# Performance work log

Hardware: AMD Instinct MI355X
Metric: run time of the kernel (lower is better)

## Reference

```python
import jax, jax.numpy as jnp
import numpy as np

B, DM, E, P, K = 8192, 512, 4, 1024, 2
F = DM * E  # fused_input_dim = 2048


def setup_inputs() -> dict:
    key = jax.random.key(0)
    ks = jax.random.split(key, 8)
    return {
        "x_mod0": jax.random.normal(ks[0], (B, DM), jnp.float32),
        "x_mod1": jax.random.normal(ks[1], (B, DM), jnp.float32),
        "x_mod2": jax.random.normal(ks[2], (B, DM), jnp.float32),
        "x_mod3": jax.random.normal(ks[3], (B, DM), jnp.float32),
        "label": jax.random.normal(ks[4], (B, P), jnp.float32),
        "Wg": jax.random.normal(ks[5], (E, F), jnp.float32) * (1.0 / np.sqrt(F)),
        "We": jax.random.normal(ks[6], (E, F, P), jnp.float32) * (1.0 / np.sqrt(F)),
        "be": jax.random.normal(ks[7], (E, P), jnp.float32) * 0.01,
        "topk": K,
    }


def reference(x_mod0, x_mod1, x_mod2, x_mod3, label, Wg, We, be, topk):
    # fused = cat(modalities, dim=1)  -> [B, F]
    fused = jnp.concatenate([x_mod0, x_mod1, x_mod2, x_mod3], axis=1)
    # gate_scores = softmax(Linear(fused))  (Linear weight is [out,in], no bias)
    gate_scores = jax.nn.softmax(fused @ Wg.T, axis=-1)  # [B, E]
    top_k_values, top_k_indices = jax.lax.top_k(gate_scores, topk)  # [B, K]
    # Dense equivalent of per-sample expert dispatch: run every expert,
    # then gather the top-k expert outputs per token and weighted-sum them.
    all_out = jnp.einsum("bf,efp->bep", fused, We) + be  # [B, E, P]
    gathered = jnp.take_along_axis(all_out, top_k_indices[:, :, None], axis=1)  # [B, K, P]
    preds = jnp.sum(gathered * top_k_values[:, :, None], axis=1)  # [B, P]
    # loss_fn = MSE against x['label']
    loss = jnp.mean((preds - label) ** 2)
    return (loss, preds)
```

## Files before the change

kernel.cpp:

```cpp
#include <hip/hip_runtime.h>
#include <stdint.h>

#define Bsz  8192
#define DMOD 512
#define NE   4
#define NP   1024
#define NF   2048
#define BM   160
#define MAXTILES 57

typedef float  f32x4  __attribute__((ext_vector_type(4)));
typedef __bf16 bf16x8 __attribute__((ext_vector_type(8)));
typedef unsigned short u16x8 __attribute__((ext_vector_type(8)));

typedef __attribute__((address_space(3))) void       lds_void;
typedef const __attribute__((address_space(1))) void glb_void;
#define GLOAD16(gp, lp) \
  __builtin_amdgcn_global_load_lds((glb_void*)(gp), (lds_void*)(lp), 16, 0, 0)

__device__ __forceinline__ unsigned short f32_bf16(float f) {
  unsigned int u = __float_as_uint(f);
  u += 0x7FFFu + ((u >> 16) & 1u);
  return (unsigned short)(u >> 16);
}

__global__ __launch_bounds__(256) void gate_kernel(
    const float* __restrict__ x0, const float* __restrict__ x1,
    const float* __restrict__ x2, const float* __restrict__ x3,
    const float* __restrict__ Wg,
    float* __restrict__ gw, int* __restrict__ pair)
{
  __shared__ float sred[4][4];
  const int b   = blockIdx.x;
  const int tid = threadIdx.x;
  const int f   = tid * 8;
  const float* xm  = (f < 1024) ? (f < 512 ? x0 : x1) : (f < 1536 ? x2 : x3);
  const float* src = xm + (size_t)b * DMOD + (f & 511);
  float4 v0 = *(const float4*)src;
  float4 v1 = *(const float4*)(src + 4);

  float d[4];
  #pragma unroll
  for (int e = 0; e < 4; ++e) {
    const float* w = Wg + e * NF + f;
    d[e] = v0.x * w[0] + v0.y * w[1] + v0.z * w[2] + v0.w * w[3]
         + v1.x * w[4] + v1.y * w[5] + v1.z * w[6] + v1.w * w[7];
  }
  #pragma unroll
  for (int off = 32; off; off >>= 1) {
    #pragma unroll
    for (int e = 0; e < 4; ++e) d[e] += __shfl_xor(d[e], off);
  }
  if ((tid & 63) == 0) {
    #pragma unroll
    for (int e = 0; e < 4; ++e) sred[tid >> 6][e] = d[e];
  }
  __syncthreads();
  if (tid == 0) {
    float a0 = sred[0][0] + sred[1][0] + sred[2][0] + sred[3][0];
    float a1 = sred[0][1] + sred[1][1] + sred[2][1] + sred[3][1];
    float a2 = sred[0][2] + sred[1][2] + sred[2][2] + sred[3][2];
    float a3 = sred[0][3] + sred[1][3] + sred[2][3] + sred[3][3];
    float m  = fmaxf(fmaxf(a0, a1), fmaxf(a2, a3));
    float e0 = expf(a0 - m), e1 = expf(a1 - m), e2 = expf(a2 - m), e3 = expf(a3 - m);
    float inv = 1.f / (e0 + e1 + e2 + e3);
    float p0 = e0 * inv, p1 = e1 * inv, p2 = e2 * inv, p3 = e3 * inv;
    int i1 = 0; float b1 = a0;
    if (a1 > b1) { b1 = a1; i1 = 1; }
    if (a2 > b1) { b1 = a2; i1 = 2; }
    if (a3 > b1) { b1 = a3; i1 = 3; }
    int i2 = -1; float b2 = -3.4e38f;
    if (i1 != 0 && a0 > b2) { b2 = a0; i2 = 0; }
    if (i1 != 1 && a1 > b2) { b2 = a1; i2 = 1; }
    if (i1 != 2 && a2 > b2) { b2 = a2; i2 = 2; }
    if (i1 != 3 && a3 > b2) { b2 = a3; i2 = 3; }
    gw[(size_t)b * 4 + 0] = (i1 == 0 || i2 == 0) ? p0 : 0.f;
    gw[(size_t)b * 4 + 1] = (i1 == 1 || i2 == 1) ? p1 : 0.f;
    gw[(size_t)b * 4 + 2] = (i1 == 2 || i2 == 2) ? p2 : 0.f;
    gw[(size_t)b * 4 + 3] = (i1 == 3 || i2 == 3) ? p3 : 0.f;
    int lo = min(i1, i2), hi = max(i1, i2);
    pair[b] = (lo == 0) ? (hi - 1) : (lo == 1) ? (hi + 1) : 5;
  }
}

__global__ __launch_bounds__(256) void we_transpose(
    const float* __restrict__ We, unsigned short* __restrict__ WeT)
{
  __shared__ float t[64][65];
  const int e  = blockIdx.z;
  const int tf = blockIdx.x * 64;
  const int tp = blockIdx.y * 64;
  const int t4 = threadIdx.x * 4;
  const float* src = We + ((size_t)e * NF + tf) * NP + tp;
  #pragma unroll
  for (int i = 0; i < 4; ++i) {
    int li = i * 1024 + t4;
    int r = li >> 6, c = li & 63;
    float4 v = *(const float4*)(src + (size_t)r * NP + c);
    t[c][r] = v.x; t[c+1][r] = v.y; t[c+2][r] = v.z; t[c+3][r] = v.w;
  }
  __syncthreads();
  unsigned short* dst = WeT + ((size_t)e * NP + tp) * NF + tf;
  #pragma unroll
  for (int i = 0; i < 4; ++i) {
    int li = i * 1024 + t4;
    int r = li >> 6, c = li & 63;
    ushort4 o;
    o.x = f32_bf16(t[r][c]);   o.y = f32_bf16(t[r][c+1]);
    o.z = f32_bf16(t[r][c+2]); o.w = f32_bf16(t[r][c+3]);
    *(ushort4*)(dst + (size_t)r * NF + c) = o;
  }
}

__global__ __launch_bounds__(256) void bucket_scan(
    const int* __restrict__ pair, int* __restrict__ ridx,
    int4* __restrict__ tiletab, int* __restrict__ ntiles,
    double* __restrict__ lossAcc)
{
  __shared__ int cntS[256][6];
  __shared__ int baseS[6];
  const int tid = threadIdx.x;
  int c[6] = {0, 0, 0, 0, 0, 0};
  for (int i = 0; i < 32; ++i) {
    const int code = pair[tid * 32 + i];
    #pragma unroll
    for (int b = 0; b < 6; ++b) c[b] += (code == b) ? 1 : 0;
  }
  #pragma unroll
  for (int b = 0; b < 6; ++b) cntS[tid][b] = c[b];
  __syncthreads();
  if (tid < 6) {
    int run = 0;
    for (int i = 0; i < 256; ++i) { const int v = cntS[i][tid]; cntS[i][tid] = run; run += v; }
    baseS[tid] = run;
  }
  __syncthreads();
  if (tid == 0) {
    const int e1t[6] = {0, 0, 0, 1, 1, 2};
    const int e2t[6] = {1, 2, 3, 2, 3, 3};
    int base[6];
    int off = 0, nt = 0;
    for (int b = 0; b < 6; ++b) {
      base[b] = off;
      const int cb = baseS[b];
      for (int i = 0; i < cb; i += BM)
        tiletab[nt++] = make_int4(off + i, min(BM, cb - i), e1t[b], e2t[b]);
      off += cb;
    }
    *ntiles = nt;
    *lossAcc = 0.0;
    #pragma unroll
    for (int b = 0; b < 6; ++b) baseS[b] = base[b];
  }
  __syncthreads();
  int pos[6];
  #pragma unroll
  for (int b = 0; b < 6; ++b) pos[b] = baseS[b] + cntS[tid][b];
  for (int i = 0; i < 32; ++i) {
    const int r = tid * 32 + i;
    const int code = pair[r];
    #pragma unroll
    for (int b = 0; b < 6; ++b)
      if (code == b) { ridx[pos[b]] = r; ++pos[b]; }
  }
}

__global__ __launch_bounds__(256) void permute_cvt(
    const float* __restrict__ x0, const float* __restrict__ x1,
    const float* __restrict__ x2, const float* __restrict__ x3,
    const int* __restrict__ ridx, unsigned short* __restrict__ fusedP)
{
  const int pos = blockIdx.x;
  const int r   = ridx[pos];
  const int tid = threadIdx.x;
  const int f   = tid * 8;
  const float* xm  = (f < 1024) ? (f < 512 ? x0 : x1) : (f < 1536 ? x2 : x3);
  const float* src = xm + (size_t)r * DMOD + (f & 511);
  float4 v0 = *(const float4*)src;
  float4 v1 = *(const float4*)(src + 4);
  u16x8 o;
  o[0] = f32_bf16(v0.x); o[1] = f32_bf16(v0.y); o[2] = f32_bf16(v0.z); o[3] = f32_bf16(v0.w);
  o[4] = f32_bf16(v1.x); o[5] = f32_bf16(v1.y); o[6] = f32_bf16(v1.z); o[7] = f32_bf16(v1.w);
  *(u16x8*)(fusedP + (size_t)pos * NF + f) = o;
}

__global__ __launch_bounds__(256, 2) void moe_gemm(
    const unsigned short* __restrict__ fusedP,
    const unsigned short* __restrict__ WeT,
    const float* __restrict__ gw,
    const float* __restrict__ be,
    const float* __restrict__ label,
    const int* __restrict__ ntilesP,
    const int4* __restrict__ tiletab,
    const int* __restrict__ ridx,
    float* __restrict__ out,
    double* __restrict__ lossAcc)
{
  const int bid  = (int)blockIdx.x;
  const int swz  = (bid & 7) * 57 + (bid >> 3);
  const int tile = swz >> 3;
  if (tile >= *ntilesP) return;
  const int pcol = (swz & 7) * 128;

  __shared__ __align__(16) unsigned short As[2][BM * 64];
  __shared__ __align__(16) unsigned short Bs[2][128 * 64];
  __shared__ int   ridxS[BM];
  __shared__ float gwS[BM][2];
  __shared__ float red[4];

  const int4 te     = tiletab[tile];
  const int rowbase = te.x;
  const int vcount  = te.y;
  const int e1      = te.z;
  const int e2      = te.w;

  const int tid  = threadIdx.x;
  const int l    = tid & 63;
  const int wave = tid >> 6;
  const int wr   = wave >> 1;
  const int wc   = wave & 1;
  const int lrow = l & 15;
  const int g4   = l >> 4;
  const int lr8  = l >> 3;
  const int lc8  = l & 7;
  const int schA = lc8 ^ lr8;

  if (tid < BM) {
    const int ri = ridx[rowbase + min(tid, vcount - 1)];
    ridxS[tid]  = ri;
    gwS[tid][0] = gw[(size_t)ri * 4 + e1];
    gwS[tid][1] = gw[(size_t)ri * 4 + e2];
  }
  __syncthreads();

  int rowA[5];
  #pragma unroll
  for (int i = 0; i < 5; ++i)
    rowA[i] = rowbase + min(wave * 40 + i * 8 + lr8, vcount - 1);

  f32x4 accT[5][4], accE[5][4];
  #pragma unroll
  for (int m = 0; m < 5; ++m)
    #pragma unroll
    for (int n = 0; n < 4; ++n) {
      accT[m][n] = f32x4{0.f, 0.f, 0.f, 0.f};
      accE[m][n] = f32x4{0.f, 0.f, 0.f, 0.f};
    }

  auto STAGE = [&](int t, int buf) {
    const int e  = (t >> 5) ? e2 : e1;
    const int k0 = (t & 31) << 6;
    const unsigned short* Bg = WeT + ((size_t)e * NP + pcol) * NF + k0;
    #pragma unroll
    for (int i = 0; i < 5; ++i) {
      const int r0 = wave * 40 + i * 8;
      GLOAD16(fusedP + (size_t)rowA[i] * NF + k0 + schA * 8, (char*)(&As[buf][r0 * 64]));
    }
    #pragma unroll
    for (int i = 0; i < 4; ++i) {
      const int r0 = wave * 32 + i * 8;
      GLOAD16(Bg + (size_t)(r0 + lr8) * NF + schA * 8, (char*)(&Bs[buf][r0 * 64]));
    }
  };

  auto COMPUTE = [&](int buf) {
    #pragma unroll
    for (int ks = 0; ks < 2; ++ks) {
      bf16x8 af[5], bfr[4];
      #pragma unroll
      for (int m = 0; m < 5; ++m) {
        const int fr = wr * 80 + m * 16 + lrow;
        const int ch = ((g4 + ks * 4) ^ (fr & 7)) * 8;
        af[m] = __builtin_bit_cast(bf16x8, *(const u16x8*)(&As[buf][fr * 64 + ch]));
      }
      #pragma unroll
      for (int n = 0; n < 4; ++n) {
        const int fr = wc * 64 + n * 16 + lrow;
        const int ch = ((g4 + ks * 4) ^ (fr & 7)) * 8;
        bfr[n] = __builtin_bit_cast(bf16x8, *(const u16x8*)(&Bs[buf][fr * 64 + ch]));
      }
      #pragma unroll
      for (int m = 0; m < 5; ++m)
        #pragma unroll
        for (int n = 0; n < 4; ++n)
          accE[m][n] = __builtin_amdgcn_mfma_f32_16x16x32_bf16(af[m], bfr[n], accE[m][n], 0, 0, 0);
    }
  };

  auto FOLD = [&](int ei) {
    #pragma unroll
    for (int m = 0; m < 5; ++m)
      #pragma unroll
      for (int r = 0; r < 4; ++r) {
        const float wv = gwS[wr * 80 + m * 16 + g4 * 4 + r][ei];
        #pragma unroll
        for (int n = 0; n < 4; ++n) {
          accT[m][n][r] += wv * accE[m][n][r];
          accE[m][n][r] = 0.f;
        }
      }
  };

  STAGE(0, 0);
  STAGE(1, 1);

  #pragma unroll 1
  for (int t = 0; t < 64; ++t) {
    const int buf = t & 1;
    if (t == 63) asm volatile("s_waitcnt vmcnt(0)" ::: "memory");
    else         asm volatile("s_waitcnt vmcnt(9)" ::: "memory");
    __builtin_amdgcn_s_barrier();
    COMPUTE(buf);
    if ((t & 31) == 31) FOLD(t >> 5);
    __builtin_amdgcn_sched_barrier(0);
    __builtin_amdgcn_s_barrier();
    if (t < 62) STAGE(t + 2, buf);
  }

  float lsum = 0.f;
  #pragma unroll
  for (int m = 0; m < 5; ++m) {
    #pragma unroll
    for (int r = 0; r < 4; ++r) {
      const int lrowi = wr * 80 + m * 16 + g4 * 4 + r;
      const bool valid = lrowi < vcount;
      const int grow = ridxS[lrowi];
      const float w1 = gwS[lrowi][0];
      const float w2 = gwS[lrowi][1];
      #pragma unroll
      for (int n = 0; n < 4; ++n) {
        const int gcol = pcol + wc * 64 + n * 16 + lrow;
        float bias = w1 * be[e1 * NP + gcol] + w2 * be[e2 * NP + gcol];
        float pred = accT[m][n][r] + bias;
        if (valid) {
          out[1 + (size_t)grow * NP + gcol] = pred;
          float d = pred - label[(size_t)grow * NP + gcol];
          lsum += d * d;
        }
      }
    }
  }
  #pragma unroll
  for (int off = 32; off; off >>= 1) lsum += __shfl_xor(lsum, off);
  if (l == 0) red[wave] = lsum;
  __syncthreads();
  if (tid == 0) {
    double s = (double)red[0] + (double)red[1] + (double)red[2] + (double)red[3];
    atomicAdd(lossAcc, s);
  }
}

__global__ void finalize_kernel(const double* __restrict__ lossAcc, float* __restrict__ out) {
  out[0] = (float)(*lossAcc * (1.0 / ((double)Bsz * (double)NP)));
}

extern "C" void kernel_launch(void* const* d_in, const int* in_sizes, int n_in,
                              void* d_out, int out_size, void* d_ws, size_t ws_size,
                              hipStream_t stream) {
  const float* x0    = (const float*)d_in[0];
  const float* x1    = (const float*)d_in[1];
  const float* x2    = (const float*)d_in[2];
  const float* x3    = (const float*)d_in[3];
  const float* label = (const float*)d_in[4];
  const float* Wg    = (const float*)d_in[5];
  const float* We    = (const float*)d_in[6];
  const float* be    = (const float*)d_in[7];
  float* out = (float*)d_out;

  char* ws = (char*)d_ws;
  unsigned short* WeT    = (unsigned short*)ws;
  unsigned short* fusedP = (unsigned short*)(ws + ((size_t)16 << 20));
  float*  gw      = (float*)(ws + ((size_t)48 << 20));
  char*   misc    = ws + ((size_t)49 << 20);
  double* lossAcc = (double*)(misc + 0);
  int*    ntiles  = (int*)(misc + 64);
  int4*   tiletab = (int4*)(misc + 256);
  int*    pair    = (int*)(misc + 4096);
  int*    ridx    = (int*)(misc + 4096 + 32768);

  gate_kernel<<<dim3(Bsz), 256, 0, stream>>>(x0, x1, x2, x3, Wg, gw, pair);
  bucket_scan<<<dim3(1), 256, 0, stream>>>(pair, ridx, tiletab, ntiles, lossAcc);
  permute_cvt<<<dim3(Bsz), 256, 0, stream>>>(x0, x1, x2, x3, ridx, fusedP);
  we_transpose<<<dim3(NF / 64, NP / 64, NE), 256, 0, stream>>>(We, WeT);
  moe_gemm<<<dim3(MAXTILES * 8), 256, 0, stream>>>(
      fusedP, WeT, gw, be, label, ntiles, tiletab, ridx, out, lossAcc);
  finalize_kernel<<<1, 1, 0, stream>>>(lossAcc, out);
}
```

Before: 171.0 us.

## Pre-scale tokens by gate weights and run single K=4096 GEMM per tile

Merges the We transpose into the gate kernel launch so both run in one grid. A new permute kernel writes two bf16 copies of each token, each pre-multiplied by one of its two gate weights. This lets the new 512-thread GEMM use one accumulator over a concatenated K of 4096 (two experts) instead of separate per-expert accumulators followed by a weighted combine. The cost is twice the permuted-activation bytes written and read, plus rounding of the scaled activations to bf16. The new path runs only when the workspace is large enough; otherwise the old pipeline is kept.

```diff
diff --git a/kernel.cpp b/kernel.cpp
--- a/kernel.cpp
+++ b/kernel.cpp
@@ -24,98 +24,99 @@
   return (unsigned short)(u >> 16);
 }
 
-__global__ __launch_bounds__(256) void gate_kernel(
+__global__ __launch_bounds__(256) void gate_tr(
     const float* __restrict__ x0, const float* __restrict__ x1,
     const float* __restrict__ x2, const float* __restrict__ x3,
-    const float* __restrict__ Wg,
-    float* __restrict__ gw, int* __restrict__ pair)
+    const float* __restrict__ Wg, const float* __restrict__ We,
+    float* __restrict__ gw, int* __restrict__ pair,
+    unsigned short* __restrict__ WeT)
 {
   __shared__ float sred[4][4];
-  const int b   = blockIdx.x;
+  __shared__ float tsh[64][65];
   const int tid = threadIdx.x;
-  const int f   = tid * 8;
-  const float* xm  = (f < 1024) ? (f < 512 ? x0 : x1) : (f < 1536 ? x2 : x3);
-  const float* src = xm + (size_t)b * DMOD + (f & 511);
-  float4 v0 = *(const float4*)src;
-  float4 v1 = *(const float4*)(src + 4);
-
-  float d[4];
-  #pragma unroll
-  for (int e = 0; e < 4; ++e) {
-    const float* w = Wg + e * NF + f;
-    d[e] = v0.x * w[0] + v0.y * w[1] + v0.z * w[2] + v0.w * w[3]
-         + v1.x * w[4] + v1.y * w[5] + v1.z * w[6] + v1.w * w[7];
-  }
-  #pragma unroll
-  for (int off = 32; off; off >>= 1) {
-    #pragma unroll
-    for (int e = 0; e < 4; ++e) d[e] += __shfl_xor(d[e], off);
-  }
-  if ((tid & 63) == 0) {
-    #pragma unroll
-    for (int e = 0; e < 4; ++e) sred[tid >> 6][e] = d[e];
-  }
-  __syncthreads();
-  if (tid == 0) {
-    float a0 = sred[0][0] + sred[1][0] + sred[2][0] + sred[3][0];
-    float a1 = sred[0][1] + sred[1][1] + sred[2][1] + sred[3][1];
-    float a2 = sred[0][2] + sred[1][2] + sred[2][2] + sred[3][2];
-    float a3 = sred[0][3] + sred[1][3] + sred[2][3] + sred[3][3];
-    float m  = fmaxf(fmaxf(a0, a1), fmaxf(a2, a3));
-    float e0 = expf(a0 - m), e1 = expf(a1 - m), e2 = expf(a2 - m), e3 = expf(a3 - m);
-    float inv = 1.f / (e0 + e1 + e2 + e3);
-    float p0 = e0 * inv, p1 = e1 * inv, p2 = e2 * inv, p3 = e3 * inv;
-    int i1 = 0; float b1 = a0;
-    if (a1 > b1) { b1 = a1; i1 = 1; }
-    if (a2 > b1) { b1 = a2; i1 = 2; }
-    if (a3 > b1) { b1 = a3; i1 = 3; }
-    int i2 = -1; float b2 = -3.4e38f;
-    if (i1 != 0 && a0 > b2) { b2 = a0; i2 = 0; }
-    if (i1 != 1 && a1 > b2) { b2 = a1; i2 = 1; }
-    if (i1 != 2 && a2 > b2) { b2 = a2; i2 = 2; }
-    if (i1 != 3 && a3 > b2) { b2 = a3; i2 = 3; }
-    gw[(size_t)b * 4 + 0] = (i1 == 0 || i2 == 0) ? p0 : 0.f;
-    gw[(size_t)b * 4 + 1] = (i1 == 1 || i2 == 1) ? p1 : 0.f;
-    gw[(size_t)b * 4 + 2] = (i1 == 2 || i2 == 2) ? p2 : 0.f;
-    gw[(size_t)b * 4 + 3] = (i1 == 3 || i2 == 3) ? p3 : 0.f;
-    int lo = min(i1, i2), hi = max(i1, i2);
-    pair[b] = (lo == 0) ? (hi - 1) : (lo == 1) ? (hi + 1) : 5;
-  }
-}
-
-__global__ __launch_bounds__(256) void we_transpose(
-    const float* __restrict__ We, unsigned short* __restrict__ WeT)
-{
-  __shared__ float t[64][65];
-  const int e  = blockIdx.z;
-  const int tf = blockIdx.x * 64;
-  const int tp = blockIdx.y * 64;
-  const int t4 = threadIdx.x * 4;
-  const float* src = We + ((size_t)e * NF + tf) * NP + tp;
-  #pragma unroll
-  for (int i = 0; i < 4; ++i) {
-    int li = i * 1024 + t4;
-    int r = li >> 6, c = li & 63;
-    float4 v = *(const float4*)(src + (size_t)r * NP + c);
-    t[c][r] = v.x; t[c+1][r] = v.y; t[c+2][r] = v.z; t[c+3][r] = v.w;
-  }
-  __syncthreads();
-  unsigned short* dst = WeT + ((size_t)e * NP + tp) * NF + tf;
-  #pragma unroll
-  for (int i = 0; i < 4; ++i) {
-    int li = i * 1024 + t4;
-    int r = li >> 6, c = li & 63;
-    ushort4 o;
-    o.x = f32_bf16(t[r][c]);   o.y = f32_bf16(t[r][c+1]);
-    o.z = f32_bf16(t[r][c+2]); o.w = f32_bf16(t[r][c+3]);
-    *(ushort4*)(dst + (size_t)r * NF + c) = o;
+
+  if ((int)blockIdx.x < Bsz) {
+    const int b = blockIdx.x;
+    const int f = tid * 8;
+    const float* xm  = (f < 1024) ? (f < 512 ? x0 : x1) : (f < 1536 ? x2 : x3);
+    const float* src = xm + (size_t)b * DMOD + (f & 511);
+    float4 v0 = *(const float4*)src;
+    float4 v1 = *(const float4*)(src + 4);
+    float d[4];
+    #pragma unroll
+    for (int e = 0; e < 4; ++e) {
+      const float* w = Wg + e * NF + f;
+      d[e] = v0.x * w[0] + v0.y * w[1] + v0.z * w[2] + v0.w * w[3]
+           + v1.x * w[4] + v1.y * w[5] + v1.z * w[6] + v1.w * w[7];
+    }
+    #pragma unroll
+    for (int off = 32; off; off >>= 1) {
+      #pragma unroll
+      for (int e = 0; e < 4; ++e) d[e] += __shfl_xor(d[e], off);
+    }
+    if ((tid & 63) == 0) {
+      #pragma unroll
+      for (int e = 0; e < 4; ++e) sred[tid >> 6][e] = d[e];
+    }
+    __syncthreads();
+    if (tid == 0) {
+      float a0 = sred[0][0] + sred[1][0] + sred[2][0] + sred[3][0];
+      float a1 = sred[0][1] + sred[1][1] + sred[2][1] + sred[3][1];
+      float a2 = sred[0][2] + sred[1][2] + sred[2][2] + sred[3][2];
+      float a3 = sred[0][3] + sred[1][3] + sred[2][3] + sred[3][3];
+      float m  = fmaxf(fmaxf(a0, a1), fmaxf(a2, a3));
+      float e0 = expf(a0 - m), e1 = expf(a1 - m), e2 = expf(a2 - m), e3 = expf(a3 - m);
+      float inv = 1.f / (e0 + e1 + e2 + e3);
+      float p0 = e0 * inv, p1 = e1 * inv, p2 = e2 * inv, p3 = e3 * inv;
+      int i1 = 0; float b1 = a0;
+      if (a1 > b1) { b1 = a1; i1 = 1; }
+      if (a2 > b1) { b1 = a2; i1 = 2; }
+      if (a3 > b1) { b1 = a3; i1 = 3; }
+      int i2 = -1; float b2 = -3.4e38f;
+      if (i1 != 0 && a0 > b2) { b2 = a0; i2 = 0; }
+      if (i1 != 1 && a1 > b2) { b2 = a1; i2 = 1; }
+      if (i1 != 2 && a2 > b2) { b2 = a2; i2 = 2; }
+      if (i1 != 3 && a3 > b2) { b2 = a3; i2 = 3; }
+      gw[(size_t)b * 4 + 0] = (i1 == 0 || i2 == 0) ? p0 : 0.f;
+      gw[(size_t)b * 4 + 1] = (i1 == 1 || i2 == 1) ? p1 : 0.f;
+      gw[(size_t)b * 4 + 2] = (i1 == 2 || i2 == 2) ? p2 : 0.f;
+      gw[(size_t)b * 4 + 3] = (i1 == 3 || i2 == 3) ? p3 : 0.f;
+      int lo = min(i1, i2), hi = max(i1, i2);
+      pair[b] = (lo == 0) ? (hi - 1) : (lo == 1) ? (hi + 1) : 5;
+    }
+  } else {
+    const int tb = (int)blockIdx.x - Bsz;
+    const int e  = tb >> 9;
+    const int rem = tb & 511;
+    const int tf = (rem & 31) * 64;
+    const int tp = (rem >> 5) * 64;
+    const int t4 = tid * 4;
+    const float* src = We + ((size_t)e * NF + tf) * NP + tp;
+    #pragma unroll
+    for (int i = 0; i < 4; ++i) {
+      int li = i * 1024 + t4;
+      int r = li >> 6, c = li & 63;
+      float4 v = *(const float4*)(src + (size_t)r * NP + c);
+      tsh[c][r] = v.x; tsh[c+1][r] = v.y; tsh[c+2][r] = v.z; tsh[c+3][r] = v.w;
+    }
+    __syncthreads();
+    unsigned short* dst = WeT + ((size_t)e * NP + tp) * NF + tf;
+    #pragma unroll
+    for (int i = 0; i < 4; ++i) {
+      int li = i * 1024 + t4;
+      int r = li >> 6, c = li & 63;
+      ushort4 o;
+      o.x = f32_bf16(tsh[r][c]);   o.y = f32_bf16(tsh[r][c+1]);
+      o.z = f32_bf16(tsh[r][c+2]); o.w = f32_bf16(tsh[r][c+3]);
+      *(ushort4*)(dst + (size_t)r * NF + c) = o;
+    }
   }
 }
 
 __global__ __launch_bounds__(256) void bucket_scan(
     const int* __restrict__ pair, int* __restrict__ ridx,
-    int4* __restrict__ tiletab, int* __restrict__ ntiles,
-    double* __restrict__ lossAcc)
+    int4* __restrict__ tiletab, int4* __restrict__ bucketTab,
+    int* __restrict__ ntiles, double* __restrict__ lossAcc)
 {
   __shared__ int cntS[256][6];
   __shared__ int baseS[6];
@@ -143,6 +144,7 @@
     for (int b = 0; b < 6; ++b) {
       base[b] = off;
       const int cb = baseS[b];
+      bucketTab[b] = make_int4(off, cb, e1t[b], e2t[b]);
       for (int i = 0; i < cb; i += BM)
         tiletab[nt++] = make_int4(off + i, min(BM, cb - i), e1t[b], e2t[b]);
       off += cb;
@@ -163,6 +165,39 @@
     for (int b = 0; b < 6; ++b)
       if (code == b) { ridx[pos[b]] = r; ++pos[b]; }
   }
+}
+
+__global__ __launch_bounds__(256) void permute_scale(
+    const float* __restrict__ x0, const float* __restrict__ x1,
+    const float* __restrict__ x2, const float* __restrict__ x3,
+    const int* __restrict__ ridx, const float* __restrict__ gw,
+    const int4* __restrict__ bucketTab, unsigned short* __restrict__ fusedP)
+{
+  const int pos = blockIdx.x;
+  int e1 = 0, e2 = 1;
+  #pragma unroll
+  for (int b = 0; b < 6; ++b) {
+    const int4 bt = bucketTab[b];
+    if (pos >= bt.x && pos < bt.x + bt.y) { e1 = bt.z; e2 = bt.w; }
+  }
+  const int ri = ridx[pos];
+  const float w1 = gw[(size_t)ri * 4 + e1];
+  const float w2 = gw[(size_t)ri * 4 + e2];
+  const int tid = threadIdx.x;
+  const int f   = tid * 8;
+  const float* xm  = (f < 1024) ? (f < 512 ? x0 : x1) : (f < 1536 ? x2 : x3);
+  const float* src = xm + (size_t)ri * DMOD + (f & 511);
+  float4 v0 = *(const float4*)src;
+  float4 v1 = *(const float4*)(src + 4);
+  float v[8] = {v0.x, v0.y, v0.z, v0.w, v1.x, v1.y, v1.z, v1.w};
+  u16x8 o1, o2;
+  #pragma unroll
+  for (int j = 0; j < 8; ++j) {
+    o1[j] = f32_bf16(v[j] * w1);
+    o2[j] = f32_bf16(v[j] * w2);
+  }
+  *(u16x8*)(fusedP + (size_t)pos * NF + f) = o1;
+  *(u16x8*)(fusedP + ((size_t)Bsz + pos) * NF + f) = o2;
 }
 
 __global__ __launch_bounds__(256) void permute_cvt(
@@ -184,7 +219,7 @@
   *(u16x8*)(fusedP + (size_t)pos * NF + f) = o;
 }
 
-__global__ __launch_bounds__(256, 2) void moe_gemm(
+__global__ __launch_bounds__(512, 4) void moe_gemm_v8(
     const unsigned short* __restrict__ fusedP,
     const unsigned short* __restrict__ WeT,
     const float* __restrict__ gw,
@@ -206,6 +241,156 @@
   __shared__ __align__(16) unsigned short Bs[2][128 * 64];
   __shared__ int   ridxS[BM];
   __shared__ float gwS[BM][2];
+  __shared__ float red[8];
+
+  const int4 te     = tiletab[tile];
+  const int rowbase = te.x;
+  const int vcount  = te.y;
+  const int e1      = te.z;
+  const int e2      = te.w;
+
+  const int tid  = threadIdx.x;
+  const int l    = tid & 63;
+  const int wave = tid >> 6;
+  const int wr   = wave >> 2;
+  const int wc   = wave & 3;
+  const int lrow = l & 15;
+  const int g4   = l >> 4;
+  const int lr8  = l >> 3;
+  const int lc8  = l & 7;
+  const int schA = lc8 ^ lr8;
+
+  if (tid < BM) {
+    const int ri = ridx[rowbase + min(tid, vcount - 1)];
+    ridxS[tid]  = ri;
+    gwS[tid][0] = gw[(size_t)ri * 4 + e1];
+    gwS[tid][1] = gw[(size_t)ri * 4 + e2];
+  }
+  __syncthreads();
+
+  f32x4 accT[5][2];
+  #pragma unroll
+  for (int m = 0; m < 5; ++m)
+    #pragma unroll
+    for (int n = 0; n < 2; ++n) accT[m][n] = f32x4{0.f, 0.f, 0.f, 0.f};
+
+  auto STAGE = [&](int t, int buf) {
+    const int h  = t >> 5;
+    const int k0 = (t & 31) << 6;
+    const unsigned short* Ag = fusedP + (size_t)h * ((size_t)Bsz * NF) + k0;
+    const unsigned short* Bg = WeT + ((size_t)(h ? e2 : e1) * NP + pcol) * NF + k0;
+    #pragma unroll
+    for (int s = 0; s < 5; ++s) {
+      if (s == 4 && wave >= 4) continue;
+      const int idx = wave + s * 8;
+      if (idx < 20) {
+        const int r0  = idx * 8;
+        const int row = rowbase + min(r0 + lr8, vcount - 1);
+        GLOAD16(Ag + (size_t)row * NF + schA * 8, (char*)(&As[buf][r0 * 64]));
+      } else {
+        const int r0 = (idx - 20) * 8;
+        GLOAD16(Bg + (size_t)(r0 + lr8) * NF + schA * 8, (char*)(&Bs[buf][r0 * 64]));
+      }
+    }
+  };
+
+  auto COMPUTE = [&](int buf) {
+    #pragma unroll
+    for (int ks = 0; ks < 2; ++ks) {
+      bf16x8 af[5], bfr[2];
+      #pragma unroll
+      for (int m = 0; m < 5; ++m) {
+        const int fr = wr * 80 + m * 16 + lrow;
+        const int ch = ((g4 + ks * 4) ^ (fr & 7)) * 8;
+        af[m] = __builtin_bit_cast(bf16x8, *(const u16x8*)(&As[buf][fr * 64 + ch]));
+      }
+      #pragma unroll
+      for (int n = 0; n < 2; ++n) {
+        const int fr = wc * 32 + n * 16 + lrow;
+        const int ch = ((g4 + ks * 4) ^ (fr & 7)) * 8;
+        bfr[n] = __builtin_bit_cast(bf16x8, *(const u16x8*)(&Bs[buf][fr * 64 + ch]));
+      }
+      #pragma unroll
+      for (int m = 0; m < 5; ++m)
+        #pragma unroll
+        for (int n = 0; n < 2; ++n)
+          accT[m][n] = __builtin_amdgcn_mfma_f32_16x16x32_bf16(af[m], bfr[n], accT[m][n], 0, 0, 0);
+    }
+  };
+
+  STAGE(0, 0);
+  STAGE(1, 1);
+
+  #pragma unroll 1
+  for (int t = 0; t < 64; ++t) {
+    const int buf = t & 1;
+    if (t == 63)          { asm volatile("s_waitcnt vmcnt(0)" ::: "memory"); }
+    else if (wave < 4)    { asm volatile("s_waitcnt vmcnt(5)" ::: "memory"); }
+    else                  { asm volatile("s_waitcnt vmcnt(4)" ::: "memory"); }
+    __builtin_amdgcn_s_barrier();
+    COMPUTE(buf);
+    __builtin_amdgcn_sched_barrier(0);
+    __builtin_amdgcn_s_barrier();
+    if (t < 62) STAGE(t + 2, buf);
+  }
+
+  float lsum = 0.f;
+  #pragma unroll
+  for (int m = 0; m < 5; ++m) {
+    #pragma unroll
+    for (int r = 0; r < 4; ++r) {
+      const int lrowi = wr * 80 + m * 16 + g4 * 4 + r;
+      const bool valid = lrowi < vcount;
+      const int grow = ridxS[lrowi];
+      const float w1 = gwS[lrowi][0];
+      const float w2 = gwS[lrowi][1];
+      #pragma unroll
+      for (int n = 0; n < 2; ++n) {
+        const int gcol = pcol + wc * 32 + n * 16 + lrow;
+        float bias = w1 * be[e1 * NP + gcol] + w2 * be[e2 * NP + gcol];
+        float pred = accT[m][n][r] + bias;
+        if (valid) {
+          out[1 + (size_t)grow * NP + gcol] = pred;
+          float d = pred - label[(size_t)grow * NP + gcol];
+          lsum += d * d;
+        }
+      }
+    }
+  }
+  #pragma unroll
+  for (int off = 32; off; off >>= 1) lsum += __shfl_xor(lsum, off);
+  if (l == 0) red[wave] = lsum;
+  __syncthreads();
+  if (tid == 0) {
+    double s = 0.0;
+    #pragma unroll
+    for (int w = 0; w < 8; ++w) s += (double)red[w];
+    atomicAdd(lossAcc, s);
+  }
+}
+
+__global__ __launch_bounds__(256, 2) void moe_gemm_r7(
+    const unsigned short* __restrict__ fusedP,
+    const unsigned short* __restrict__ WeT,
+    const float* __restrict__ gw,
+    const float* __restrict__ be,
+    const float* __restrict__ label,
+    const int* __restrict__ ntilesP,
+    const int4* __restrict__ tiletab,
+    const int* __restrict__ ridx,
+    float* __restrict__ out,
+    double* __restrict__ lossAcc)
+{
+  const int bid  = (int)blockIdx.x;
+  const int swz  = (bid & 7) * 57 + (bid >> 3);
+  const int tile = swz >> 3;
+  if (tile >= *ntilesP) return;
+  const int pcol = (swz & 7) * 128;
+
+  __shared__ __align__(16) unsigned short As[2][BM * 64];
+  __shared__ __align__(16) unsigned short Bs[2][128 * 64];
+  __shared__ int   ridxS[BM];
+  __shared__ float gwS[BM][2];
   __shared__ float red[4];
 
   const int4 te     = tiletab[tile];
@@ -366,23 +551,45 @@
   const float* We    = (const float*)d_in[6];
   const float* be    = (const float*)d_in[7];
   float* out = (float*)d_out;
-
   char* ws = (char*)d_ws;
-  unsigned short* WeT    = (unsigned short*)ws;
-  unsigned short* fusedP = (unsigned short*)(ws + ((size_t)16 << 20));
-  float*  gw      = (float*)(ws + ((size_t)48 << 20));
-  char*   misc    = ws + ((size_t)49 << 20);
-  double* lossAcc = (double*)(misc + 0);
-  int*    ntiles  = (int*)(misc + 64);
-  int4*   tiletab = (int4*)(misc + 256);
-  int*    pair    = (int*)(misc + 4096);
-  int*    ridx    = (int*)(misc + 4096 + 32768);
-
-  gate_kernel<<<dim3(Bsz), 256, 0, stream>>>(x0, x1, x2, x3, Wg, gw, pair);
-  bucket_scan<<<dim3(1), 256, 0, stream>>>(pair, ridx, tiletab, ntiles, lossAcc);
-  permute_cvt<<<dim3(Bsz), 256, 0, stream>>>(x0, x1, x2, x3, ridx, fusedP);
-  we_transpose<<<dim3(NF / 64, NP / 64, NE), 256, 0, stream>>>(We, WeT);
-  moe_gemm<<<dim3(MAXTILES * 8), 256, 0, stream>>>(
-      fusedP, WeT, gw, be, label, ntiles, tiletab, ridx, out, lossAcc);
-  finalize_kernel<<<1, 1, 0, stream>>>(lossAcc, out);
-}
+
+  const bool bigWs = ws_size >= ((size_t)82 << 20);
+
+  if (bigWs) {
+    unsigned short* WeT    = (unsigned short*)ws;
+    unsigned short* fusedP = (unsigned short*)(ws + ((size_t)16 << 20));
+    char*   misc    = ws + ((size_t)80 << 20);
+    double* lossAcc = (double*)(misc + 0);
+    int*    ntiles  = (int*)(misc + 64);
+    int4*   tiletab = (int4*)(misc + 256);
+    int4*   bucketTab = (int4*)(misc + 2048);
+    int*    pair    = (int*)(misc + 4096);
+    int*    ridx    = (int*)(misc + 4096 + 32768);
+    float*  gw      = (float*)(misc + 4096 + 65536);
+
+    gate_tr<<<dim3(Bsz + 2048), 256, 0, stream>>>(x0, x1, x2, x3, Wg, We, gw, pair, WeT);
+    bucket_scan<<<dim3(1), 256, 0, stream>>>(pair, ridx, tiletab, bucketTab, ntiles, lossAcc);
+    permute_scale<<<dim3(Bsz), 256, 0, stream>>>(x0, x1, x2, x3, ridx, gw, bucketTab, fusedP);
+    moe_gemm_v8<<<dim3(MAXTILES * 8), 512, 0, stream>>>(
+        fusedP, WeT, gw, be, label, ntiles, tiletab, ridx, out, lossAcc);
+    finalize_kernel<<<1, 1, 0, stream>>>(lossAcc, out);
+  } else {
+    unsigned short* WeT    = (unsigned short*)ws;
+    unsigned short* fusedP = (unsigned short*)(ws + ((size_t)16 << 20));
+    float*  gw      = (float*)(ws + ((size_t)48 << 20));
+    char*   misc    = ws + ((size_t)49 << 20);
+    double* lossAcc = (double*)(misc + 0);
+    int*    ntiles  = (int*)(misc + 64);
+    int4*   tiletab = (int4*)(misc + 256);
+    int4*   bucketTab = (int4*)(misc + 2048);
+    int*    pair    = (int*)(misc + 4096);
+    int*    ridx    = (int*)(misc + 4096 + 32768);
+
+    gate_tr<<<dim3(Bsz + 2048), 256, 0, stream>>>(x0, x1, x2, x3, Wg, We, gw, pair, WeT);
+    bucket_scan<<<dim3(1), 256, 0, stream>>>(pair, ridx, tiletab, bucketTab, ntiles, lossAcc);
+    permute_cvt<<<dim3(Bsz), 256, 0, stream>>>(x0, x1, x2, x3, ridx, fusedP);
+    moe_gemm_r7<<<dim3(MAXTILES * 8), 256, 0, stream>>>(
+        fusedP, WeT, gw, be, label, ntiles, tiletab, ridx, out, lossAcc);
+    finalize_kernel<<<1, 1, 0, stream>>>(lossAcc, out);
+  }
+}
```

Result: faster. 161.2 us (-5.7%).

## Fuse gate, bf16 conversion and We transpose; compute both experts concurrently in GEMM

Applied to the files above, without the earlier changes.

The gate kernel, the activation bf16 conversion and the We transpose now run as one launch, and the separate permute kernel is removed. The GEMM now gathers rows through ridx directly from the unpermuted bf16 activations. The GEMM moves to 512 threads with K-step 32 and keeps two accumulator sets, one per expert, each multiplied against the same A fragment. This replaces the sequential two-expert K loop and its fold step. The aim is to cut launches and a full activation copy and to reuse A loads across both experts, at the cost of doubled B traffic per step, scattered row reads and a different pipeline depth.

```diff
diff --git a/kernel.cpp b/kernel.cpp
--- a/kernel.cpp
+++ b/kernel.cpp
@@ -24,91 +24,97 @@
   return (unsigned short)(u >> 16);
 }
 
-__global__ __launch_bounds__(256) void gate_kernel(
+__global__ __launch_bounds__(256) void gate_fuse(
     const float* __restrict__ x0, const float* __restrict__ x1,
     const float* __restrict__ x2, const float* __restrict__ x3,
-    const float* __restrict__ Wg,
-    float* __restrict__ gw, int* __restrict__ pair)
+    const float* __restrict__ Wg, const float* __restrict__ We,
+    float* __restrict__ gw, int* __restrict__ pair,
+    unsigned short* __restrict__ fusedB, unsigned short* __restrict__ WeT)
 {
   __shared__ float sred[4][4];
-  const int b   = blockIdx.x;
+  __shared__ float tsh[64][65];
   const int tid = threadIdx.x;
-  const int f   = tid * 8;
-  const float* xm  = (f < 1024) ? (f < 512 ? x0 : x1) : (f < 1536 ? x2 : x3);
-  const float* src = xm + (size_t)b * DMOD + (f & 511);
-  float4 v0 = *(const float4*)src;
-  float4 v1 = *(const float4*)(src + 4);
-
-  float d[4];
-  #pragma unroll
-  for (int e = 0; e < 4; ++e) {
-    const float* w = Wg + e * NF + f;
-    d[e] = v0.x * w[0] + v0.y * w[1] + v0.z * w[2] + v0.w * w[3]
-         + v1.x * w[4] + v1.y * w[5] + v1.z * w[6] + v1.w * w[7];
-  }
-  #pragma unroll
-  for (int off = 32; off; off >>= 1) {
-    #pragma unroll
-    for (int e = 0; e < 4; ++e) d[e] += __shfl_xor(d[e], off);
-  }
-  if ((tid & 63) == 0) {
-    #pragma unroll
-    for (int e = 0; e < 4; ++e) sred[tid >> 6][e] = d[e];
-  }
-  __syncthreads();
-  if (tid == 0) {
-    float a0 = sred[0][0] + sred[1][0] + sred[2][0] + sred[3][0];
-    float a1 = sred[0][1] + sred[1][1] + sred[2][1] + sred[3][1];
-    float a2 = sred[0][2] + sred[1][2] + sred[2][2] + sred[3][2];
-    float a3 = sred[0][3] + sred[1][3] + sred[2][3] + sred[3][3];
-    float m  = fmaxf(fmaxf(a0, a1), fmaxf(a2, a3));
-    float e0 = expf(a0 - m), e1 = expf(a1 - m), e2 = expf(a2 - m), e3 = expf(a3 - m);
-    float inv = 1.f / (e0 + e1 + e2 + e3);
-    float p0 = e0 * inv, p1 = e1 * inv, p2 = e2 * inv, p3 = e3 * inv;
-    int i1 = 0; float b1 = a0;
-    if (a1 > b1) { b1 = a1; i1 = 1; }
-    if (a2 > b1) { b1 = a2; i1 = 2; }
-    if (a3 > b1) { b1 = a3; i1 = 3; }
-    int i2 = -1; float b2 = -3.4e38f;
-    if (i1 != 0 && a0 > b2) { b2 = a0; i2 = 0; }
-    if (i1 != 1 && a1 > b2) { b2 = a1; i2 = 1; }
-    if (i1 != 2 && a2 > b2) { b2 = a2; i2 = 2; }
-    if (i1 != 3 && a3 > b2) { b2 = a3; i2 = 3; }
-    gw[(size_t)b * 4 + 0] = (i1 == 0 || i2 == 0) ? p0 : 0.f;
-    gw[(size_t)b * 4 + 1] = (i1 == 1 || i2 == 1) ? p1 : 0.f;
-    gw[(size_t)b * 4 + 2] = (i1 == 2 || i2 == 2) ? p2 : 0.f;
-    gw[(size_t)b * 4 + 3] = (i1 == 3 || i2 == 3) ? p3 : 0.f;
-    int lo = min(i1, i2), hi = max(i1, i2);
-    pair[b] = (lo == 0) ? (hi - 1) : (lo == 1) ? (hi + 1) : 5;
-  }
-}
-
-__global__ __launch_bounds__(256) void we_transpose(
-    const float* __restrict__ We, unsigned short* __restrict__ WeT)
-{
-  __shared__ float t[64][65];
-  const int e  = blockIdx.z;
-  const int tf = blockIdx.x * 64;
-  const int tp = blockIdx.y * 64;
-  const int t4 = threadIdx.x * 4;
-  const float* src = We + ((size_t)e * NF + tf) * NP + tp;
-  #pragma unroll
-  for (int i = 0; i < 4; ++i) {
-    int li = i * 1024 + t4;
-    int r = li >> 6, c = li & 63;
-    float4 v = *(const float4*)(src + (size_t)r * NP + c);
-    t[c][r] = v.x; t[c+1][r] = v.y; t[c+2][r] = v.z; t[c+3][r] = v.w;
-  }
-  __syncthreads();
-  unsigned short* dst = WeT + ((size_t)e * NP + tp) * NF + tf;
-  #pragma unroll
-  for (int i = 0; i < 4; ++i) {
-    int li = i * 1024 + t4;
-    int r = li >> 6, c = li & 63;
-    ushort4 o;
-    o.x = f32_bf16(t[r][c]);   o.y = f32_bf16(t[r][c+1]);
-    o.z = f32_bf16(t[r][c+2]); o.w = f32_bf16(t[r][c+3]);
-    *(ushort4*)(dst + (size_t)r * NF + c) = o;
+
+  if ((int)blockIdx.x < Bsz) {
+    const int b = blockIdx.x;
+    const int f = tid * 8;
+    const float* xm  = (f < 1024) ? (f < 512 ? x0 : x1) : (f < 1536 ? x2 : x3);
+    const float* src = xm + (size_t)b * DMOD + (f & 511);
+    float4 v0 = *(const float4*)src;
+    float4 v1 = *(const float4*)(src + 4);
+    u16x8 o;
+    o[0] = f32_bf16(v0.x); o[1] = f32_bf16(v0.y); o[2] = f32_bf16(v0.z); o[3] = f32_bf16(v0.w);
+    o[4] = f32_bf16(v1.x); o[5] = f32_bf16(v1.y); o[6] = f32_bf16(v1.z); o[7] = f32_bf16(v1.w);
+    *(u16x8*)(fusedB + (size_t)b * NF + f) = o;
+
+    float d[4];
+    #pragma unroll
+    for (int e = 0; e < 4; ++e) {
+      const float* w = Wg + e * NF + f;
+      d[e] = v0.x * w[0] + v0.y * w[1] + v0.z * w[2] + v0.w * w[3]
+           + v1.x * w[4] + v1.y * w[5] + v1.z * w[6] + v1.w * w[7];
+    }
+    #pragma unroll
+    for (int off = 32; off; off >>= 1) {
+      #pragma unroll
+      for (int e = 0; e < 4; ++e) d[e] += __shfl_xor(d[e], off);
+    }
+    if ((tid & 63) == 0) {
+      #pragma unroll
+      for (int e = 0; e < 4; ++e) sred[tid >> 6][e] = d[e];
+    }
+    __syncthreads();
+    if (tid == 0) {
+      float a0 = sred[0][0] + sred[1][0] + sred[2][0] + sred[3][0];
+      float a1 = sred[0][1] + sred[1][1] + sred[2][1] + sred[3][1];
+      float a2 = sred[0][2] + sred[1][2] + sred[2][2] + sred[3][2];
+      float a3 = sred[0][3] + sred[1][3] + sred[2][3] + sred[3][3];
+      float m  = fmaxf(fmaxf(a0, a1), fmaxf(a2, a3));
+      float e0 = expf(a0 - m), e1 = expf(a1 - m), e2 = expf(a2 - m), e3 = expf(a3 - m);
+      float inv = 1.f / (e0 + e1 + e2 + e3);
+      float p0 = e0 * inv, p1 = e1 * inv, p2 = e2 * inv, p3 = e3 * inv;
+      int i1 = 0; float b1 = a0;
+      if (a1 > b1) { b1 = a1; i1 = 1; }
+      if (a2 > b1) { b1 = a2; i1 = 2; }
+      if (a3 > b1) { b1 = a3; i1 = 3; }
+      int i2 = -1; float b2 = -3.4e38f;
+      if (i1 != 0 && a0 > b2) { b2 = a0; i2 = 0; }
+      if (i1 != 1 && a1 > b2) { b2 = a1; i2 = 1; }
+      if (i1 != 2 && a2 > b2) { b2 = a2; i2 = 2; }
+      if (i1 != 3 && a3 > b2) { b2 = a3; i2 = 3; }
+      gw[(size_t)b * 4 + 0] = (i1 == 0 || i2 == 0) ? p0 : 0.f;
+      gw[(size_t)b * 4 + 1] = (i1 == 1 || i2 == 1) ? p1 : 0.f;
+      gw[(size_t)b * 4 + 2] = (i1 == 2 || i2 == 2) ? p2 : 0.f;
+      gw[(size_t)b * 4 + 3] = (i1 == 3 || i2 == 3) ? p3 : 0.f;
+      int lo = min(i1, i2), hi = max(i1, i2);
+      pair[b] = (lo == 0) ? (hi - 1) : (lo == 1) ? (hi + 1) : 5;
+    }
+  } else {
+    const int tb = (int)blockIdx.x - Bsz;
+    const int e  = tb >> 9;
+    const int rem = tb & 511;
+    const int tf = (rem & 31) * 64;
+    const int tp = (rem >> 5) * 64;
+    const int t4 = tid * 4;
+    const float* src = We + ((size_t)e * NF + tf) * NP + tp;
+    #pragma unroll
+    for (int i = 0; i < 4; ++i) {
+      int li = i * 1024 + t4;
+      int r = li >> 6, c = li & 63;
+      float4 v = *(const float4*)(src + (size_t)r * NP + c);
+      tsh[c][r] = v.x; tsh[c+1][r] = v.y; tsh[c+2][r] = v.z; tsh[c+3][r] = v.w;
+    }
+    __syncthreads();
+    unsigned short* dst = WeT + ((size_t)e * NP + tp) * NF + tf;
+    #pragma unroll
+    for (int i = 0; i < 4; ++i) {
+      int li = i * 1024 + t4;
+      int r = li >> 6, c = li & 63;
+      ushort4 o;
+      o.x = f32_bf16(tsh[r][c]);   o.y = f32_bf16(tsh[r][c+1]);
+      o.z = f32_bf16(tsh[r][c+2]); o.w = f32_bf16(tsh[r][c+3]);
+      *(ushort4*)(dst + (size_t)r * NF + c) = o;
+    }
   }
 }
 
@@ -165,27 +171,8 @@
   }
 }
 
-__global__ __launch_bounds__(256) void permute_cvt(
-    const float* __restrict__ x0, const float* __restrict__ x1,
-    const float* __restrict__ x2, const float* __restrict__ x3,
-    const int* __restrict__ ridx, unsigned short* __restrict__ fusedP)
-{
-  const int pos = blockIdx.x;
-  const int r   = ridx[pos];
-  const int tid = threadIdx.x;
-  const int f   = tid * 8;
-  const float* xm  = (f < 1024) ? (f < 512 ? x0 : x1) : (f < 1536 ? x2 : x3);
-  const float* src = xm + (size_t)r * DMOD + (f & 511);
-  float4 v0 = *(const float4*)src;
-  float4 v1 = *(const float4*)(src + 4);
-  u16x8 o;
-  o[0] = f32_bf16(v0.x); o[1] = f32_bf16(v0.y); o[2] = f32_bf16(v0.z); o[3] = f32_bf16(v0.w);
-  o[4] = f32_bf16(v1.x); o[5] = f32_bf16(v1.y); o[6] = f32_bf16(v1.z); o[7] = f32_bf16(v1.w);
-  *(u16x8*)(fusedP + (size_t)pos * NF + f) = o;
-}
-
-__global__ __launch_bounds__(256, 2) void moe_gemm(
-    const unsigned short* __restrict__ fusedP,
+__global__ __launch_bounds__(512, 4) void moe_gemm_db(
+    const unsigned short* __restrict__ fusedB,
     const unsigned short* __restrict__ WeT,
     const float* __restrict__ gw,
     const float* __restrict__ be,
@@ -202,11 +189,12 @@
   if (tile >= *ntilesP) return;
   const int pcol = (swz & 7) * 128;
 
-  __shared__ __align__(16) unsigned short As[2][BM * 64];
-  __shared__ __align__(16) unsigned short Bs[2][128 * 64];
+  __shared__ __align__(16) unsigned short As[2][BM * 32];
+  __shared__ __align__(16) unsigned short B1s[2][128 * 32];
+  __shared__ __align__(16) unsigned short B2s[2][128 * 32];
   __shared__ int   ridxS[BM];
   __shared__ float gwS[BM][2];
-  __shared__ float red[4];
+  __shared__ float red[8];
 
   const int4 te     = tiletab[tile];
   const int rowbase = te.x;
@@ -217,13 +205,11 @@
   const int tid  = threadIdx.x;
   const int l    = tid & 63;
   const int wave = tid >> 6;
-  const int wr   = wave >> 1;
-  const int wc   = wave & 1;
+  const int wr   = wave >> 2;
+  const int wc   = wave & 3;
   const int lrow = l & 15;
   const int g4   = l >> 4;
-  const int lr8  = l >> 3;
-  const int lc8  = l & 7;
-  const int schA = lc8 ^ lr8;
+  const int schA = (l & 3) ^ ((l >> 3) & 3);
 
   if (tid < BM) {
     const int ri = ridx[rowbase + min(tid, vcount - 1)];
@@ -233,71 +219,61 @@
   }
   __syncthreads();
 
-  int rowA[5];
-  #pragma unroll
-  for (int i = 0; i < 5; ++i)
-    rowA[i] = rowbase + min(wave * 40 + i * 8 + lr8, vcount - 1);
-
-  f32x4 accT[5][4], accE[5][4];
+  const int rowA0 = ridxS[wave * 16 + (l >> 2)];
+  const int rowA1 = (wave < 2) ? ridxS[(8 + wave) * 16 + (l >> 2)] : 0;
+
+  f32x4 acc1[5][2], acc2[5][2];
   #pragma unroll
   for (int m = 0; m < 5; ++m)
     #pragma unroll
-    for (int n = 0; n < 4; ++n) {
-      accT[m][n] = f32x4{0.f, 0.f, 0.f, 0.f};
-      accE[m][n] = f32x4{0.f, 0.f, 0.f, 0.f};
+    for (int n = 0; n < 2; ++n) {
+      acc1[m][n] = f32x4{0.f, 0.f, 0.f, 0.f};
+      acc2[m][n] = f32x4{0.f, 0.f, 0.f, 0.f};
     }
 
   auto STAGE = [&](int t, int buf) {
-    const int e  = (t >> 5) ? e2 : e1;
-    const int k0 = (t & 31) << 6;
-    const unsigned short* Bg = WeT + ((size_t)e * NP + pcol) * NF + k0;
-    #pragma unroll
-    for (int i = 0; i < 5; ++i) {
-      const int r0 = wave * 40 + i * 8;
-      GLOAD16(fusedP + (size_t)rowA[i] * NF + k0 + schA * 8, (char*)(&As[buf][r0 * 64]));
-    }
-    #pragma unroll
-    for (int i = 0; i < 4; ++i) {
-      const int r0 = wave * 32 + i * 8;
-      GLOAD16(Bg + (size_t)(r0 + lr8) * NF + schA * 8, (char*)(&Bs[buf][r0 * 64]));
+    const int k0 = t << 5;
+    const unsigned short* B1g = WeT + ((size_t)e1 * NP + pcol) * NF + k0;
+    const unsigned short* B2g = WeT + ((size_t)e2 * NP + pcol) * NF + k0;
+    #pragma unroll
+    for (int s = 0; s < 4; ++s) {
+      const int idx = wave + s * 8;
+      if (idx >= 26) continue;
+      if (idx < 10) {
+        const int r0  = idx * 16;
+        const int row = (s == 0) ? rowA0 : rowA1;
+        GLOAD16(fusedB + (size_t)row * NF + k0 + schA * 8, (char*)(&As[buf][r0 * 32]));
+      } else if (idx < 18) {
+        const int r0 = (idx - 10) * 16;
+        GLOAD16(B1g + (size_t)(r0 + (l >> 2)) * NF + schA * 8, (char*)(&B1s[buf][r0 * 32]));
+      } else {
+        const int r0 = (idx - 18) * 16;
+        GLOAD16(B2g + (size_t)(r0 + (l >> 2)) * NF + schA * 8, (char*)(&B2s[buf][r0 * 32]));
+      }
     }
   };
 
   auto COMPUTE = [&](int buf) {
-    #pragma unroll
-    for (int ks = 0; ks < 2; ++ks) {
-      bf16x8 af[5], bfr[4];
-      #pragma unroll
-      for (int m = 0; m < 5; ++m) {
-        const int fr = wr * 80 + m * 16 + lrow;
-        const int ch = ((g4 + ks * 4) ^ (fr & 7)) * 8;
-        af[m] = __builtin_bit_cast(bf16x8, *(const u16x8*)(&As[buf][fr * 64 + ch]));
-      }
-      #pragma unroll
-      for (int n = 0; n < 4; ++n) {
-        const int fr = wc * 64 + n * 16 + lrow;
-        const int ch = ((g4 + ks * 4) ^ (fr & 7)) * 8;
-        bfr[n] = __builtin_bit_cast(bf16x8, *(const u16x8*)(&Bs[buf][fr * 64 + ch]));
-      }
-      #pragma unroll
-      for (int m = 0; m < 5; ++m)
-        #pragma unroll
-        for (int n = 0; n < 4; ++n)
-          accE[m][n] = __builtin_amdgcn_mfma_f32_16x16x32_bf16(af[m], bfr[n], accE[m][n], 0, 0, 0);
-    }
-  };
-
-  auto FOLD = [&](int ei) {
+    bf16x8 af[5], b1f[2], b2f[2];
+    #pragma unroll
+    for (int m = 0; m < 5; ++m) {
+      const int fr = wr * 80 + m * 16 + lrow;
+      const int ch = (g4 ^ ((fr >> 1) & 3)) * 8;
+      af[m] = __builtin_bit_cast(bf16x8, *(const u16x8*)(&As[buf][fr * 32 + ch]));
+    }
+    #pragma unroll
+    for (int n = 0; n < 2; ++n) {
+      const int fr = wc * 32 + n * 16 + lrow;
+      const int ch = (g4 ^ ((fr >> 1) & 3)) * 8;
+      b1f[n] = __builtin_bit_cast(bf16x8, *(const u16x8*)(&B1s[buf][fr * 32 + ch]));
+      b2f[n] = __builtin_bit_cast(bf16x8, *(const u16x8*)(&B2s[buf][fr * 32 + ch]));
+    }
     #pragma unroll
     for (int m = 0; m < 5; ++m)
       #pragma unroll
-      for (int r = 0; r < 4; ++r) {
-        const float wv = gwS[wr * 80 + m * 16 + g4 * 4 + r][ei];
-        #pragma unroll
-        for (int n = 0; n < 4; ++n) {
-          accT[m][n][r] += wv * accE[m][n][r];
-          accE[m][n][r] = 0.f;
-        }
+      for (int n = 0; n < 2; ++n) {
+        acc1[m][n] = __builtin_amdgcn_mfma_f32_16x16x32_bf16(af[m], b1f[n], acc1[m][n], 0, 0, 0);
+        acc2[m][n] = __builtin_amdgcn_mfma_f32_16x16x32_bf16(af[m], b2f[n], acc2[m][n], 0, 0, 0);
       }
   };
 
@@ -307,11 +283,11 @@
   #pragma unroll 1
   for (int t = 0; t < 64; ++t) {
     const int buf = t & 1;
-    if (t == 63) asm volatile("s_waitcnt vmcnt(0)" ::: "memory");
-    else         asm volatile("s_waitcnt vmcnt(9)" ::: "memory");
+    if (t == 63)       { asm volatile("s_waitcnt vmcnt(0)" ::: "memory"); }
+    else if (wave < 2) { asm volatile("s_waitcnt vmcnt(4)" ::: "memory"); }
+    else               { asm volatile("s_waitcnt vmcnt(3)" ::: "memory"); }
     __builtin_amdgcn_s_barrier();
     COMPUTE(buf);
-    if ((t & 31) == 31) FOLD(t >> 5);
     __builtin_amdgcn_sched_barrier(0);
     __builtin_amdgcn_s_barrier();
     if (t < 62) STAGE(t + 2, buf);
@@ -328,10 +304,10 @@
       const float w1 = gwS[lrowi][0];
       const float w2 = gwS[lrowi][1];
       #pragma unroll
-      for (int n = 0; n < 4; ++n) {
-        const int gcol = pcol + wc * 64 + n * 16 + lrow;
-        float bias = w1 * be[e1 * NP + gcol] + w2 * be[e2 * NP + gcol];
-        float pred = accT[m][n][r] + bias;
+      for (int n = 0; n < 2; ++n) {
+        const int gcol = pcol + wc * 32 + n * 16 + lrow;
+        float pred = w1 * (acc1[m][n][r] + be[e1 * NP + gcol])
+                   + w2 * (acc2[m][n][r] + be[e2 * NP + gcol]);
         if (valid) {
           out[1 + (size_t)grow * NP + gcol] = pred;
           float d = pred - label[(size_t)grow * NP + gcol];
@@ -345,7 +321,9 @@
   if (l == 0) red[wave] = lsum;
   __syncthreads();
   if (tid == 0) {
-    double s = (double)red[0] + (double)red[1] + (double)red[2] + (double)red[3];
+    double s = 0.0;
+    #pragma unroll
+    for (int w = 0; w < 8; ++w) s += (double)red[w];
     atomicAdd(lossAcc, s);
   }
 }
@@ -369,7 +347,7 @@
 
   char* ws = (char*)d_ws;
   unsigned short* WeT    = (unsigned short*)ws;
-  unsigned short* fusedP = (unsigned short*)(ws + ((size_t)16 << 20));
+  unsigned short* fusedB = (unsigned short*)(ws + ((size_t)16 << 20));
   float*  gw      = (float*)(ws + ((size_t)48 << 20));
   char*   misc    = ws + ((size_t)49 << 20);
   double* lossAcc = (double*)(misc + 0);
@@ -378,11 +356,9 @@
   int*    pair    = (int*)(misc + 4096);
   int*    ridx    = (int*)(misc + 4096 + 32768);
 
-  gate_kernel<<<dim3(Bsz), 256, 0, stream>>>(x0, x1, x2, x3, Wg, gw, pair);
+  gate_fuse<<<dim3(Bsz + 2048), 256, 0, stream>>>(x0, x1, x2, x3, Wg, We, gw, pair, fusedB, WeT);
   bucket_scan<<<dim3(1), 256, 0, stream>>>(pair, ridx, tiletab, ntiles, lossAcc);
-  permute_cvt<<<dim3(Bsz), 256, 0, stream>>>(x0, x1, x2, x3, ridx, fusedP);
-  we_transpose<<<dim3(NF / 64, NP / 64, NE), 256, 0, stream>>>(We, WeT);
-  moe_gemm<<<dim3(MAXTILES * 8), 256, 0, stream>>>(
-      fusedP, WeT, gw, be, label, ntiles, tiletab, ridx, out, lossAcc);
+  moe_gemm_db<<<dim3(MAXTILES * 8), 512, 0, stream>>>(
+      fusedB, WeT, gw, be, label, ntiles, tiletab, ridx, out, lossAcc);
   finalize_kernel<<<1, 1, 0, stream>>>(lossAcc, out);
 }
```

After: 141.7 us. 1.21x faster.
